# Performance work log

Measured on AMD Instinct MI355X. Metric: run time of the kernel, lower is better.

Reference implementation:

```python
import jax, jax.numpy as jnp
import numpy as np

B, N, D, R = 4, 2048, 1024, 64
LN_EPS = 1e-5


def setup_inputs() -> dict:
    key = jax.random.key(0)
    k_x, k_m, k_u, k_v = jax.random.split(key, 4)
    x = jax.random.normal(k_x, (B, N, D), dtype=jnp.float32)
    mask = jax.random.uniform(k_m, (B, N, R), dtype=jnp.float32)
    # xavier-style init for low-rank bases U_max, V_max: (d_model, R_max)
    scale = jnp.sqrt(2.0 / (D + R)).astype(jnp.float32)
    U = jax.random.normal(k_u, (D, R), dtype=jnp.float32) * scale
    V = jax.random.normal(k_v, (D, R), dtype=jnp.float32) * scale
    gamma = jnp.ones((D,), dtype=jnp.float32)
    beta = jnp.zeros((D,), dtype=jnp.float32)
    return {"x": x, "mask": mask, "U": U, "V": V, "gamma": gamma, "beta": beta}


def _layernorm(y, gamma, beta):
    mu = jnp.mean(y, axis=-1, keepdims=True)
    var = jnp.mean(jnp.square(y - mu), axis=-1, keepdims=True)
    return (y - mu) * jax.lax.rsqrt(var + LN_EPS) * gamma + beta


def reference(x, mask, U, V, gamma, beta):
    # Q/K: low-rank projections gated by per-token continuous mask
    Q = jnp.einsum('bnd,dr->bnr', x, U) * mask            # (B, N, R)
    K = jnp.einsum('bnd,dr->bnr', x, V) * mask            # (B, N, R)
    # effective rank per query token, clamped at 1
    r_eff = jnp.maximum(jnp.sum(mask, axis=-1, keepdims=True), 1.0)  # (B, N, 1)
    scores = jnp.einsum('bqr,bkr->bqk', Q, K) / jnp.sqrt(r_eff)      # (B, N, N)
    A = jax.nn.softmax(scores, axis=-1)
    delta = jnp.einsum('bqk,bkd->bqd', A, x)              # (B, N, D)
    # backbone is identity: out = LN(x + delta)
    return _layernorm(x + delta, gamma, beta)
```

## Files before the change

kernel.cpp:

```cpp
#include <hip/hip_runtime.h>

#define Bb 4
#define Nn 2048
#define Dd 1024
#define Rr 64
#define LN_EPS 1e-5f

typedef unsigned short u16;
typedef short bf16x8 __attribute__((ext_vector_type(8)));
typedef float f32x4 __attribute__((ext_vector_type(4)));

__device__ __forceinline__ u16 f2bf(float f) {
  unsigned u = __float_as_uint(f);
  u += 0x7FFFu + ((u >> 16) & 1u);
  return (u16)(u >> 16);
}

__device__ __forceinline__ void g2l16(u16* l, const u16* g) {
  __builtin_amdgcn_global_load_lds(
      (const __attribute__((address_space(1))) unsigned int*)g,
      (__attribute__((address_space(3))) unsigned int*)l, 16, 0, 0);
}

__global__ __launch_bounds__(256) void prep_x(const float* __restrict__ x,
                                              u16* __restrict__ xt) {
  __shared__ float tile[64][65];
  const int b = blockIdx.z;
  const int n0 = blockIdx.x * 64;
  const int d0 = blockIdx.y * 64;
  const int t = threadIdx.x;
  const int c = t & 63, r4 = t >> 6;
#pragma unroll
  for (int rr = 0; rr < 16; rr++) {
    int row = rr * 4 + r4;
    tile[row][c] = x[(size_t)(b * Nn + n0 + row) * Dd + d0 + c];
  }
  __syncthreads();
#pragma unroll
  for (int rr = 0; rr < 16; rr++) {
    int dd = rr * 4 + r4;
    xt[(size_t)(b * Dd + d0 + dd) * Nn + n0 + c] = f2bf(tile[c][dd]);
  }
}

__global__ __launch_bounds__(256) void prep_small(const float* __restrict__ U,
    const float* __restrict__ V, const float* __restrict__ mask,
    u16* __restrict__ uvt, float* __restrict__ qs) {
  if (blockIdx.x < 32) {
    __shared__ float tile[64][65];
    const int which = blockIdx.x >> 4;
    const int d0 = (blockIdx.x & 15) * 64;
    const float* src = which ? V : U;
    const int t = threadIdx.x, c = t & 63, r4 = t >> 6;
#pragma unroll
    for (int rr = 0; rr < 16; rr++) {
      int row = rr * 4 + r4;
      tile[row][c] = src[(size_t)(d0 + row) * Rr + c];
    }
    __syncthreads();
#pragma unroll
    for (int rr = 0; rr < 16; rr++) {
      int r = rr * 4 + r4;
      uvt[(size_t)(which * 64 + r) * Dd + d0 + c] = f2bf(tile[c][r]);
    }
  } else {
    const int row = (blockIdx.x - 32) * 4 + (threadIdx.x >> 6);
    const int lane = threadIdx.x & 63;
    float v = mask[(size_t)row * Rr + lane];
#pragma unroll
    for (int off = 32; off; off >>= 1) v += __shfl_xor(v, off);
    if (lane == 0) qs[row] = rsqrtf(fmaxf(v, 1.0f));
  }
}

__global__ __launch_bounds__(256) void proj_qk(const float* __restrict__ x,
    const float* __restrict__ mask, const u16* __restrict__ uvt,
    const float* __restrict__ qs,
    u16* __restrict__ Qo, u16* __restrict__ Ko) {
  const int t = threadIdx.x;
  const int w = t >> 6, l = t & 63, quad = l >> 4, l16 = l & 15;
  const int g0 = blockIdx.x * 32;
  f32x4 acc[2][2];
#pragma unroll
  for (int i = 0; i < 2; i++)
#pragma unroll
    for (int j = 0; j < 2; j++) acc[i][j] = (f32x4){0.f, 0.f, 0.f, 0.f};
  for (int k0 = 0; k0 < Dd; k0 += 32) {
    bf16x8 a[2];
#pragma unroll
    for (int mt = 0; mt < 2; mt++) {
      const float4* px = (const float4*)&x[(size_t)(g0 + mt * 16 + l16) * Dd + k0 + quad * 8];
      float4 x0 = px[0], x1 = px[1];
      bf16x8 av;
      av[0] = (short)f2bf(x0.x); av[1] = (short)f2bf(x0.y);
      av[2] = (short)f2bf(x0.z); av[3] = (short)f2bf(x0.w);
      av[4] = (short)f2bf(x1.x); av[5] = (short)f2bf(x1.y);
      av[6] = (short)f2bf(x1.z); av[7] = (short)f2bf(x1.w);
      a[mt] = av;
    }
    bf16x8 bfr[2];
#pragma unroll
    for (int i = 0; i < 2; i++) {
      int col = (w * 2 + i) * 16 + l16;
      bfr[i] = *(const bf16x8*)&uvt[(size_t)col * Dd + k0 + quad * 8];
    }
#pragma unroll
    for (int mt = 0; mt < 2; mt++)
#pragma unroll
      for (int i = 0; i < 2; i++)
        acc[mt][i] = __builtin_amdgcn_mfma_f32_16x16x32_bf16(a[mt], bfr[i], acc[mt][i], 0, 0, 0);
  }
#pragma unroll
  for (int mt = 0; mt < 2; mt++)
#pragma unroll
    for (int i = 0; i < 2; i++) {
      int col = (w * 2 + i) * 16 + l16;
      int r_ = col & 63;
#pragma unroll
      for (int r = 0; r < 4; r++) {
        int row = g0 + mt * 16 + quad * 4 + r;
        float v = acc[mt][i][r] * mask[(size_t)row * Rr + r_];
        if (col < 64) Qo[(size_t)row * Rr + r_] = f2bf(v * qs[row]);
        else          Ko[(size_t)row * Rr + r_] = f2bf(v);
      }
    }
}

__global__ __launch_bounds__(512, 2) void score_softmax(
    const u16* __restrict__ Qm, const u16* __restrict__ Km,
    u16* __restrict__ Pw, float* __restrict__ linv_g) {
  __shared__ float red[32][8];
  __shared__ float mfin[32];
  __shared__ u16 tsl[8][32][80];
  const int t = threadIdx.x;
  const int w = t >> 6, l = t & 63, quad = l >> 4, l16 = l & 15;
  const int id = blockIdx.x;
  const int xcd = id & 7;
  const int b = xcd >> 1;
  const int q0 = (((id >> 3) << 1) | (xcd & 1)) * 32;
  bf16x8 qf[2][2];
#pragma unroll
  for (int mt = 0; mt < 2; mt++)
#pragma unroll
    for (int ks = 0; ks < 2; ks++)
      qf[mt][ks] = *(const bf16x8*)&Qm[(size_t)(b * Nn + q0 + mt * 16 + l16) * Rr + ks * 32 + quad * 8];
  f32x4 acc[2][16];
#pragma unroll
  for (int mt = 0; mt < 2; mt++)
#pragma unroll
    for (int nt = 0; nt < 16; nt++) acc[mt][nt] = (f32x4){0.f, 0.f, 0.f, 0.f};
#pragma unroll
  for (int nt = 0; nt < 16; nt++) {
#pragma unroll
    for (int ks = 0; ks < 2; ks++) {
      bf16x8 kf = *(const bf16x8*)&Km[(size_t)(b * Nn + w * 256 + nt * 16 + l16) * Rr + ks * 32 + quad * 8];
#pragma unroll
      for (int mt = 0; mt < 2; mt++)
        acc[mt][nt] = __builtin_amdgcn_mfma_f32_16x16x32_bf16(qf[mt][ks], kf, acc[mt][nt], 0, 0, 0);
    }
  }
  float vmax[2][4];
#pragma unroll
  for (int mt = 0; mt < 2; mt++)
#pragma unroll
    for (int r = 0; r < 4; r++) {
      float m = -1e30f;
#pragma unroll
      for (int nt = 0; nt < 16; nt++) m = fmaxf(m, acc[mt][nt][r]);
#pragma unroll
      for (int off = 1; off < 16; off <<= 1) m = fmaxf(m, __shfl_xor(m, off));
      vmax[mt][r] = m;
    }
  if (l16 == 0) {
#pragma unroll
    for (int mt = 0; mt < 2; mt++)
#pragma unroll
      for (int r = 0; r < 4; r++) red[mt * 16 + quad * 4 + r][w] = vmax[mt][r];
  }
  __syncthreads();
  if (t < 32) {
    float m = -1e30f;
#pragma unroll
    for (int i = 0; i < 8; i++) m = fmaxf(m, red[t][i]);
    mfin[t] = m;
  }
  __syncthreads();
  float rowm[2][4], vsum[2][4];
#pragma unroll
  for (int mt = 0; mt < 2; mt++)
#pragma unroll
    for (int r = 0; r < 4; r++) {
      rowm[mt][r] = mfin[mt * 16 + quad * 4 + r];
      vsum[mt][r] = 0.f;
    }
#pragma unroll
  for (int mt = 0; mt < 2; mt++)
#pragma unroll
    for (int nt = 0; nt < 16; nt++)
#pragma unroll
      for (int r = 0; r < 4; r++) {
        float p = __expf(acc[mt][nt][r] - rowm[mt][r]);
        acc[mt][nt][r] = p;
        vsum[mt][r] += p;
      }
#pragma unroll
  for (int mt = 0; mt < 2; mt++)
#pragma unroll
    for (int r = 0; r < 4; r++) {
#pragma unroll
      for (int off = 1; off < 16; off <<= 1) vsum[mt][r] += __shfl_xor(vsum[mt][r], off);
    }
  __syncthreads();
  if (l16 == 0) {
#pragma unroll
    for (int mt = 0; mt < 2; mt++)
#pragma unroll
      for (int r = 0; r < 4; r++) red[mt * 16 + quad * 4 + r][w] = vsum[mt][r];
  }
  __syncthreads();
  if (t < 32) {
    float s = 0.f;
#pragma unroll
    for (int i = 0; i < 8; i++) s += red[t][i];
    linv_g[(size_t)b * Nn + q0 + t] = 1.f / s;
  }
#pragma unroll
  for (int c = 0; c < 4; c++) {
#pragma unroll
    for (int mt = 0; mt < 2; mt++)
#pragma unroll
      for (int i = 0; i < 4; i++) {
        const int nt = c * 4 + i;
#pragma unroll
        for (int r = 0; r < 4; r++)
          tsl[w][mt * 16 + quad * 4 + r][i * 16 + l16] = f2bf(acc[mt][nt][r]);
      }
#pragma unroll
    for (int it = 0; it < 4; it++) {
      const int u = it * 64 + l;
      const int row = u >> 3, cg = u & 7;
      bf16x8 vv = *(const bf16x8*)&tsl[w][row][cg * 8];
      *(bf16x8*)&Pw[((size_t)(b * Nn + q0 + row)) * Nn + w * 256 + c * 64 + cg * 8] = vv;
    }
  }
}

__global__ __launch_bounds__(256, 2) void pv_gemm(
    const u16* __restrict__ Pw, const u16* __restrict__ xt,
    const float* __restrict__ x, const float* __restrict__ linv_g,
    float* __restrict__ y) {
  __shared__ u16 As[128 * 64];
  __shared__ u16 Bs[128 * 64];
  const int t = threadIdx.x;
  const int w = t >> 6, l = t & 63, quad = l >> 4, l16 = l & 15;
  const int id = blockIdx.x;
  const int xcd = id & 7;
  const int b = xcd >> 1;
  const int nh = xcd & 1;
  const int rest = id >> 3;
  const int m0 = (rest & 15) * 128;
  const int n0 = (nh * 4 + (rest >> 4)) * 128;
  const int srow = w * 32 + (l >> 3);
  const int skoff = (((l & 7) ^ ((l >> 3) & 7)) * 8);
  f32x4 acc[4][4];
#pragma unroll
  for (int i = 0; i < 4; i++)
#pragma unroll
    for (int j = 0; j < 4; j++) acc[i][j] = (f32x4){0.f, 0.f, 0.f, 0.f};
  const int wm = w & 1, wn = w >> 1;
  const int sw = (l16 & 7);
  for (int k0 = 0; k0 < Nn; k0 += 64) {
    __syncthreads();
#pragma unroll
    for (int c = 0; c < 4; c++) {
      int row = srow + c * 8;
      g2l16(&As[(w * 32 + c * 8) * 64],
            &Pw[((size_t)(b * Nn + m0 + row)) * Nn + k0 + skoff]);
      g2l16(&Bs[(w * 32 + c * 8) * 64],
            &xt[((size_t)(b * Dd + n0 + row)) * Nn + k0 + skoff]);
    }
    __syncthreads();
#pragma unroll
    for (int ks = 0; ks < 2; ks++) {
      const int slot = ((ks * 4 + quad) ^ sw) * 8;
      bf16x8 af[4], bf_[4];
#pragma unroll
      for (int mt = 0; mt < 4; mt++)
        af[mt] = *(const bf16x8*)&As[(wm * 64 + mt * 16 + l16) * 64 + slot];
#pragma unroll
      for (int nt = 0; nt < 4; nt++)
        bf_[nt] = *(const bf16x8*)&Bs[(wn * 64 + nt * 16 + l16) * 64 + slot];
#pragma unroll
      for (int mt = 0; mt < 4; mt++)
#pragma unroll
        for (int nt = 0; nt < 4; nt++)
          acc[mt][nt] = __builtin_amdgcn_mfma_f32_16x16x32_bf16(af[mt], bf_[nt], acc[mt][nt], 0, 0, 0);
    }
  }
  float li[4][4];
#pragma unroll
  for (int mt = 0; mt < 4; mt++)
#pragma unroll
    for (int r = 0; r < 4; r++)
      li[mt][r] = linv_g[(size_t)b * Nn + m0 + wm * 64 + mt * 16 + quad * 4 + r];
#pragma unroll
  for (int mt = 0; mt < 4; mt++)
#pragma unroll
    for (int nt = 0; nt < 4; nt++) {
      const int nn = n0 + wn * 64 + nt * 16 + l16;
#pragma unroll
      for (int r = 0; r < 4; r++) {
        const int m = m0 + wm * 64 + mt * 16 + quad * 4 + r;
        const size_t off = ((size_t)(b * Nn + m)) * Dd + nn;
        y[off] = x[off] + li[mt][r] * acc[mt][nt][r];
      }
    }
}

__global__ __launch_bounds__(256) void ln_k(float* __restrict__ y,
    const float* __restrict__ gamma, const float* __restrict__ beta) {
  __shared__ float rs[4], rq[4];
  const int row = blockIdx.x;
  const int t = threadIdx.x;
  float* p = y + (size_t)row * Dd;
  float4 v = ((const float4*)p)[t];
  float s = v.x + v.y + v.z + v.w;
  float q = v.x * v.x + v.y * v.y + v.z * v.z + v.w * v.w;
#pragma unroll
  for (int off = 32; off; off >>= 1) {
    s += __shfl_xor(s, off);
    q += __shfl_xor(q, off);
  }
  if ((t & 63) == 0) { rs[t >> 6] = s; rq[t >> 6] = q; }
  __syncthreads();
  float S = rs[0] + rs[1] + rs[2] + rs[3];
  float Q2 = rq[0] + rq[1] + rq[2] + rq[3];
  float mu = S * (1.f / Dd);
  float var = Q2 * (1.f / Dd) - mu * mu;
  float rstd = rsqrtf(var + LN_EPS);
  float4 g = ((const float4*)gamma)[t];
  float4 be = ((const float4*)beta)[t];
  v.x = (v.x - mu) * rstd * g.x + be.x;
  v.y = (v.y - mu) * rstd * g.y + be.y;
  v.z = (v.z - mu) * rstd * g.z + be.z;
  v.w = (v.w - mu) * rstd * g.w + be.w;
  ((float4*)p)[t] = v;
}

extern "C" void kernel_launch(void* const* d_in, const int* in_sizes, int n_in,
                              void* d_out, int out_size, void* d_ws, size_t ws_size,
                              hipStream_t stream) {
  const float* x     = (const float*)d_in[0];
  const float* mask  = (const float*)d_in[1];
  const float* U     = (const float*)d_in[2];
  const float* V     = (const float*)d_in[3];
  const float* gamma = (const float*)d_in[4];
  const float* beta  = (const float*)d_in[5];
  float* out = (float*)d_out;
  char* ws = (char*)d_ws;
  u16*   xt   = (u16*)ws;
  u16*   Qw   = (u16*)(ws + (size_t)(16 << 20));
  u16*   Kw   = (u16*)(ws + (size_t)(17 << 20));
  u16*   uvt  = (u16*)(ws + (size_t)(18 << 20));
  float* qsb  = (float*)(ws + (size_t)(18 << 20) + (256 << 10));
  float* linv = (float*)(ws + (size_t)(18 << 20) + (288 << 10));
  u16*   Pw   = (u16*)(ws + (size_t)(19 << 20));

  prep_x       <<<dim3(Nn / 64, Dd / 64, Bb), 256, 0, stream>>>(x, xt);
  prep_small   <<<32 + (Bb * Nn) / 4, 256, 0, stream>>>(U, V, mask, uvt, qsb);
  proj_qk      <<<(Bb * Nn) / 32, 256, 0, stream>>>(x, mask, uvt, qsb, Qw, Kw);
  score_softmax<<<Bb * (Nn / 32), 512, 0, stream>>>(Qw, Kw, Pw, linv);
  pv_gemm      <<<Bb * (Nn / 128) * (Dd / 128), 256, 0, stream>>>(Pw, xt, x, linv, out);
  ln_k         <<<Bb * Nn, 256, 0, stream>>>(out, gamma, beta);
}
```

Measured before the change: 191.8 us.

## Shrink row tiles in projection and softmax, fuse qs into proj, one-wave LayerNorm rows

The mask row-sum and rsqrt scale move from a separate prep kernel into proj_qk, which now handles 16 rows per block and double-buffers its x and U/V register loads. score_softmax drops to 16 query rows per block with launch bounds raised to 4 blocks per CU, which lowers register pressure and doubles the block count. LayerNorm now assigns one wave per row and four rows per block, so the shared-memory reduction and block barrier are gone. The goal is more parallelism and occupancy in the small kernels and one fewer pass. The cost is that K fragments are reloaded from memory twice as often and grids get larger.

```diff
diff --git a/kernel.cpp b/kernel.cpp
--- a/kernel.cpp
+++ b/kernel.cpp
@@ -43,182 +43,166 @@
   }
 }
 
-__global__ __launch_bounds__(256) void prep_small(const float* __restrict__ U,
-    const float* __restrict__ V, const float* __restrict__ mask,
-    u16* __restrict__ uvt, float* __restrict__ qs) {
-  if (blockIdx.x < 32) {
-    __shared__ float tile[64][65];
-    const int which = blockIdx.x >> 4;
-    const int d0 = (blockIdx.x & 15) * 64;
-    const float* src = which ? V : U;
-    const int t = threadIdx.x, c = t & 63, r4 = t >> 6;
-#pragma unroll
-    for (int rr = 0; rr < 16; rr++) {
-      int row = rr * 4 + r4;
-      tile[row][c] = src[(size_t)(d0 + row) * Rr + c];
-    }
-    __syncthreads();
-#pragma unroll
-    for (int rr = 0; rr < 16; rr++) {
-      int r = rr * 4 + r4;
-      uvt[(size_t)(which * 64 + r) * Dd + d0 + c] = f2bf(tile[c][r]);
-    }
-  } else {
-    const int row = (blockIdx.x - 32) * 4 + (threadIdx.x >> 6);
-    const int lane = threadIdx.x & 63;
-    float v = mask[(size_t)row * Rr + lane];
-#pragma unroll
-    for (int off = 32; off; off >>= 1) v += __shfl_xor(v, off);
-    if (lane == 0) qs[row] = rsqrtf(fmaxf(v, 1.0f));
+__global__ __launch_bounds__(256) void prep_uv(const float* __restrict__ U,
+    const float* __restrict__ V, u16* __restrict__ uvt) {
+  __shared__ float tile[64][65];
+  const int which = blockIdx.x >> 4;
+  const int d0 = (blockIdx.x & 15) * 64;
+  const float* src = which ? V : U;
+  const int t = threadIdx.x, c = t & 63, r4 = t >> 6;
+#pragma unroll
+  for (int rr = 0; rr < 16; rr++) {
+    int row = rr * 4 + r4;
+    tile[row][c] = src[(size_t)(d0 + row) * Rr + c];
+  }
+  __syncthreads();
+#pragma unroll
+  for (int rr = 0; rr < 16; rr++) {
+    int r = rr * 4 + r4;
+    uvt[(size_t)(which * 64 + r) * Dd + d0 + c] = f2bf(tile[c][r]);
   }
 }
 
 __global__ __launch_bounds__(256) void proj_qk(const float* __restrict__ x,
     const float* __restrict__ mask, const u16* __restrict__ uvt,
-    const float* __restrict__ qs,
     u16* __restrict__ Qo, u16* __restrict__ Ko) {
+  __shared__ float qsl[16];
   const int t = threadIdx.x;
   const int w = t >> 6, l = t & 63, quad = l >> 4, l16 = l & 15;
-  const int g0 = blockIdx.x * 32;
-  f32x4 acc[2][2];
-#pragma unroll
-  for (int i = 0; i < 2; i++)
-#pragma unroll
-    for (int j = 0; j < 2; j++) acc[i][j] = (f32x4){0.f, 0.f, 0.f, 0.f};
+  const int g0 = blockIdx.x * 16;
+#pragma unroll
+  for (int it = 0; it < 4; it++) {
+    const int row = it * 4 + w;
+    float v = mask[(size_t)(g0 + row) * Rr + l];
+#pragma unroll
+    for (int off = 32; off; off >>= 1) v += __shfl_xor(v, off);
+    if (l == 0) qsl[row] = rsqrtf(fmaxf(v, 1.0f));
+  }
+  f32x4 acc[2];
+  acc[0] = (f32x4){0.f, 0.f, 0.f, 0.f};
+  acc[1] = (f32x4){0.f, 0.f, 0.f, 0.f};
+  bf16x8 a_cur, b_cur[2];
+  {
+    const float4* px = (const float4*)&x[(size_t)(g0 + l16) * Dd + quad * 8];
+    float4 x0 = px[0], x1 = px[1];
+    a_cur[0] = (short)f2bf(x0.x); a_cur[1] = (short)f2bf(x0.y);
+    a_cur[2] = (short)f2bf(x0.z); a_cur[3] = (short)f2bf(x0.w);
+    a_cur[4] = (short)f2bf(x1.x); a_cur[5] = (short)f2bf(x1.y);
+    a_cur[6] = (short)f2bf(x1.z); a_cur[7] = (short)f2bf(x1.w);
+#pragma unroll
+    for (int i = 0; i < 2; i++) {
+      int col = w * 32 + i * 16 + l16;
+      b_cur[i] = *(const bf16x8*)&uvt[(size_t)col * Dd + quad * 8];
+    }
+  }
   for (int k0 = 0; k0 < Dd; k0 += 32) {
-    bf16x8 a[2];
-#pragma unroll
-    for (int mt = 0; mt < 2; mt++) {
-      const float4* px = (const float4*)&x[(size_t)(g0 + mt * 16 + l16) * Dd + k0 + quad * 8];
+    const int k1 = (k0 + 32 < Dd) ? k0 + 32 : 0;
+    bf16x8 a_nxt, b_nxt[2];
+    {
+      const float4* px = (const float4*)&x[(size_t)(g0 + l16) * Dd + k1 + quad * 8];
       float4 x0 = px[0], x1 = px[1];
-      bf16x8 av;
-      av[0] = (short)f2bf(x0.x); av[1] = (short)f2bf(x0.y);
-      av[2] = (short)f2bf(x0.z); av[3] = (short)f2bf(x0.w);
-      av[4] = (short)f2bf(x1.x); av[5] = (short)f2bf(x1.y);
-      av[6] = (short)f2bf(x1.z); av[7] = (short)f2bf(x1.w);
-      a[mt] = av;
-    }
-    bf16x8 bfr[2];
-#pragma unroll
-    for (int i = 0; i < 2; i++) {
-      int col = (w * 2 + i) * 16 + l16;
-      bfr[i] = *(const bf16x8*)&uvt[(size_t)col * Dd + k0 + quad * 8];
-    }
-#pragma unroll
-    for (int mt = 0; mt < 2; mt++)
-#pragma unroll
-      for (int i = 0; i < 2; i++)
-        acc[mt][i] = __builtin_amdgcn_mfma_f32_16x16x32_bf16(a[mt], bfr[i], acc[mt][i], 0, 0, 0);
-  }
-#pragma unroll
-  for (int mt = 0; mt < 2; mt++)
-#pragma unroll
-    for (int i = 0; i < 2; i++) {
-      int col = (w * 2 + i) * 16 + l16;
-      int r_ = col & 63;
-#pragma unroll
-      for (int r = 0; r < 4; r++) {
-        int row = g0 + mt * 16 + quad * 4 + r;
-        float v = acc[mt][i][r] * mask[(size_t)row * Rr + r_];
-        if (col < 64) Qo[(size_t)row * Rr + r_] = f2bf(v * qs[row]);
-        else          Ko[(size_t)row * Rr + r_] = f2bf(v);
+      a_nxt[0] = (short)f2bf(x0.x); a_nxt[1] = (short)f2bf(x0.y);
+      a_nxt[2] = (short)f2bf(x0.z); a_nxt[3] = (short)f2bf(x0.w);
+      a_nxt[4] = (short)f2bf(x1.x); a_nxt[5] = (short)f2bf(x1.y);
+      a_nxt[6] = (short)f2bf(x1.z); a_nxt[7] = (short)f2bf(x1.w);
+#pragma unroll
+      for (int i = 0; i < 2; i++) {
+        int col = w * 32 + i * 16 + l16;
+        b_nxt[i] = *(const bf16x8*)&uvt[(size_t)col * Dd + k1 + quad * 8];
       }
     }
-}
-
-__global__ __launch_bounds__(512, 2) void score_softmax(
+#pragma unroll
+    for (int i = 0; i < 2; i++)
+      acc[i] = __builtin_amdgcn_mfma_f32_16x16x32_bf16(a_cur, b_cur[i], acc[i], 0, 0, 0);
+    a_cur = a_nxt; b_cur[0] = b_nxt[0]; b_cur[1] = b_nxt[1];
+  }
+  __syncthreads();
+#pragma unroll
+  for (int i = 0; i < 2; i++) {
+    const int col = w * 32 + i * 16 + l16;
+    const int r_ = col & 63;
+#pragma unroll
+    for (int r = 0; r < 4; r++) {
+      const int rl = quad * 4 + r;
+      const int row = g0 + rl;
+      float v = acc[i][r] * mask[(size_t)row * Rr + r_];
+      if (col < 64) Qo[(size_t)row * Rr + r_] = f2bf(v * qsl[rl]);
+      else          Ko[(size_t)row * Rr + r_] = f2bf(v);
+    }
+  }
+}
+
+__global__ __launch_bounds__(512, 4) void score_softmax(
     const u16* __restrict__ Qm, const u16* __restrict__ Km,
     u16* __restrict__ Pw, float* __restrict__ linv_g) {
-  __shared__ float red[32][8];
-  __shared__ float mfin[32];
-  __shared__ u16 tsl[8][32][80];
+  __shared__ float red[16][8];
+  __shared__ float mfin[16];
+  __shared__ u16 tsl[8][16][72];
   const int t = threadIdx.x;
   const int w = t >> 6, l = t & 63, quad = l >> 4, l16 = l & 15;
   const int id = blockIdx.x;
   const int xcd = id & 7;
   const int b = xcd >> 1;
-  const int q0 = (((id >> 3) << 1) | (xcd & 1)) * 32;
-  bf16x8 qf[2][2];
-#pragma unroll
-  for (int mt = 0; mt < 2; mt++)
-#pragma unroll
-    for (int ks = 0; ks < 2; ks++)
-      qf[mt][ks] = *(const bf16x8*)&Qm[(size_t)(b * Nn + q0 + mt * 16 + l16) * Rr + ks * 32 + quad * 8];
-  f32x4 acc[2][16];
-#pragma unroll
-  for (int mt = 0; mt < 2; mt++)
-#pragma unroll
-    for (int nt = 0; nt < 16; nt++) acc[mt][nt] = (f32x4){0.f, 0.f, 0.f, 0.f};
+  const int q0 = (((id >> 3) << 1) | (xcd & 1)) * 16;
+  bf16x8 qf[2];
+#pragma unroll
+  for (int ks = 0; ks < 2; ks++)
+    qf[ks] = *(const bf16x8*)&Qm[(size_t)(b * Nn + q0 + l16) * Rr + ks * 32 + quad * 8];
+  f32x4 acc[16];
+#pragma unroll
+  for (int nt = 0; nt < 16; nt++) acc[nt] = (f32x4){0.f, 0.f, 0.f, 0.f};
 #pragma unroll
   for (int nt = 0; nt < 16; nt++) {
 #pragma unroll
     for (int ks = 0; ks < 2; ks++) {
       bf16x8 kf = *(const bf16x8*)&Km[(size_t)(b * Nn + w * 256 + nt * 16 + l16) * Rr + ks * 32 + quad * 8];
-#pragma unroll
-      for (int mt = 0; mt < 2; mt++)
-        acc[mt][nt] = __builtin_amdgcn_mfma_f32_16x16x32_bf16(qf[mt][ks], kf, acc[mt][nt], 0, 0, 0);
-    }
-  }
-  float vmax[2][4];
-#pragma unroll
-  for (int mt = 0; mt < 2; mt++)
-#pragma unroll
-    for (int r = 0; r < 4; r++) {
-      float m = -1e30f;
-#pragma unroll
-      for (int nt = 0; nt < 16; nt++) m = fmaxf(m, acc[mt][nt][r]);
-#pragma unroll
-      for (int off = 1; off < 16; off <<= 1) m = fmaxf(m, __shfl_xor(m, off));
-      vmax[mt][r] = m;
-    }
+      acc[nt] = __builtin_amdgcn_mfma_f32_16x16x32_bf16(qf[ks], kf, acc[nt], 0, 0, 0);
+    }
+  }
+  float vmax[4];
+#pragma unroll
+  for (int r = 0; r < 4; r++) {
+    float m = -1e30f;
+#pragma unroll
+    for (int nt = 0; nt < 16; nt++) m = fmaxf(m, acc[nt][r]);
+#pragma unroll
+    for (int off = 1; off < 16; off <<= 1) m = fmaxf(m, __shfl_xor(m, off));
+    vmax[r] = m;
+  }
   if (l16 == 0) {
 #pragma unroll
-    for (int mt = 0; mt < 2; mt++)
-#pragma unroll
-      for (int r = 0; r < 4; r++) red[mt * 16 + quad * 4 + r][w] = vmax[mt][r];
-  }
-  __syncthreads();
-  if (t < 32) {
+    for (int r = 0; r < 4; r++) red[quad * 4 + r][w] = vmax[r];
+  }
+  __syncthreads();
+  if (t < 16) {
     float m = -1e30f;
 #pragma unroll
     for (int i = 0; i < 8; i++) m = fmaxf(m, red[t][i]);
     mfin[t] = m;
   }
   __syncthreads();
-  float rowm[2][4], vsum[2][4];
-#pragma unroll
-  for (int mt = 0; mt < 2; mt++)
+  float rowm[4], vsum[4];
+#pragma unroll
+  for (int r = 0; r < 4; r++) { rowm[r] = mfin[quad * 4 + r]; vsum[r] = 0.f; }
+#pragma unroll
+  for (int nt = 0; nt < 16; nt++)
 #pragma unroll
     for (int r = 0; r < 4; r++) {
-      rowm[mt][r] = mfin[mt * 16 + quad * 4 + r];
-      vsum[mt][r] = 0.f;
-    }
-#pragma unroll
-  for (int mt = 0; mt < 2; mt++)
-#pragma unroll
-    for (int nt = 0; nt < 16; nt++)
-#pragma unroll
-      for (int r = 0; r < 4; r++) {
-        float p = __expf(acc[mt][nt][r] - rowm[mt][r]);
-        acc[mt][nt][r] = p;
-        vsum[mt][r] += p;
-      }
-#pragma unroll
-  for (int mt = 0; mt < 2; mt++)
-#pragma unroll
-    for (int r = 0; r < 4; r++) {
-#pragma unroll
-      for (int off = 1; off < 16; off <<= 1) vsum[mt][r] += __shfl_xor(vsum[mt][r], off);
-    }
-  __syncthreads();
+      float p = __expf(acc[nt][r] - rowm[r]);
+      acc[nt][r] = p;
+      vsum[r] += p;
+    }
+#pragma unroll
+  for (int r = 0; r < 4; r++) {
+#pragma unroll
+    for (int off = 1; off < 16; off <<= 1) vsum[r] += __shfl_xor(vsum[r], off);
+  }
   if (l16 == 0) {
 #pragma unroll
-    for (int mt = 0; mt < 2; mt++)
-#pragma unroll
-      for (int r = 0; r < 4; r++) red[mt * 16 + quad * 4 + r][w] = vsum[mt][r];
-  }
-  __syncthreads();
-  if (t < 32) {
+    for (int r = 0; r < 4; r++) red[quad * 4 + r][w] = vsum[r];
+  }
+  __syncthreads();
+  if (t < 16) {
     float s = 0.f;
 #pragma unroll
     for (int i = 0; i < 8; i++) s += red[t][i];
@@ -227,16 +211,14 @@
 #pragma unroll
   for (int c = 0; c < 4; c++) {
 #pragma unroll
-    for (int mt = 0; mt < 2; mt++)
-#pragma unroll
-      for (int i = 0; i < 4; i++) {
-        const int nt = c * 4 + i;
-#pragma unroll
-        for (int r = 0; r < 4; r++)
-          tsl[w][mt * 16 + quad * 4 + r][i * 16 + l16] = f2bf(acc[mt][nt][r]);
-      }
-#pragma unroll
-    for (int it = 0; it < 4; it++) {
+    for (int i = 0; i < 4; i++) {
+      const int nt = c * 4 + i;
+#pragma unroll
+      for (int r = 0; r < 4; r++)
+        tsl[w][quad * 4 + r][i * 16 + l16] = f2bf(acc[nt][r]);
+    }
+#pragma unroll
+    for (int it = 0; it < 2; it++) {
       const int u = it * 64 + l;
       const int row = u >> 3, cg = u & 7;
       bf16x8 vv = *(const bf16x8*)&tsl[w][row][cg * 8];
@@ -319,32 +301,36 @@
 
 __global__ __launch_bounds__(256) void ln_k(float* __restrict__ y,
     const float* __restrict__ gamma, const float* __restrict__ beta) {
-  __shared__ float rs[4], rq[4];
-  const int row = blockIdx.x;
-  const int t = threadIdx.x;
+  const int t = threadIdx.x, w = t >> 6, lane = t & 63;
+  const int row = blockIdx.x * 4 + w;
   float* p = y + (size_t)row * Dd;
-  float4 v = ((const float4*)p)[t];
-  float s = v.x + v.y + v.z + v.w;
-  float q = v.x * v.x + v.y * v.y + v.z * v.z + v.w * v.w;
+  float4 v[4];
+  float s = 0.f, q = 0.f;
+#pragma unroll
+  for (int i = 0; i < 4; i++) {
+    v[i] = ((const float4*)p)[i * 64 + lane];
+    s += v[i].x + v[i].y + v[i].z + v[i].w;
+    q += v[i].x * v[i].x + v[i].y * v[i].y + v[i].z * v[i].z + v[i].w * v[i].w;
+  }
 #pragma unroll
   for (int off = 32; off; off >>= 1) {
     s += __shfl_xor(s, off);
     q += __shfl_xor(q, off);
   }
-  if ((t & 63) == 0) { rs[t >> 6] = s; rq[t >> 6] = q; }
-  __syncthreads();
-  float S = rs[0] + rs[1] + rs[2] + rs[3];
-  float Q2 = rq[0] + rq[1] + rq[2] + rq[3];
-  float mu = S * (1.f / Dd);
-  float var = Q2 * (1.f / Dd) - mu * mu;
-  float rstd = rsqrtf(var + LN_EPS);
-  float4 g = ((const float4*)gamma)[t];
-  float4 be = ((const float4*)beta)[t];
-  v.x = (v.x - mu) * rstd * g.x + be.x;
-  v.y = (v.y - mu) * rstd * g.y + be.y;
-  v.z = (v.z - mu) * rstd * g.z + be.z;
-  v.w = (v.w - mu) * rstd * g.w + be.w;
-  ((float4*)p)[t] = v;
+  const float mu = s * (1.f / Dd);
+  const float var = q * (1.f / Dd) - mu * mu;
+  const float rstd = rsqrtf(var + LN_EPS);
+#pragma unroll
+  for (int i = 0; i < 4; i++) {
+    float4 g = ((const float4*)gamma)[i * 64 + lane];
+    float4 be = ((const float4*)beta)[i * 64 + lane];
+    float4 o;
+    o.x = (v[i].x - mu) * rstd * g.x + be.x;
+    o.y = (v[i].y - mu) * rstd * g.y + be.y;
+    o.z = (v[i].z - mu) * rstd * g.z + be.z;
+    o.w = (v[i].w - mu) * rstd * g.w + be.w;
+    ((float4*)p)[i * 64 + lane] = o;
+  }
 }
 
 extern "C" void kernel_launch(void* const* d_in, const int* in_sizes, int n_in,
@@ -362,14 +348,13 @@
   u16*   Qw   = (u16*)(ws + (size_t)(16 << 20));
   u16*   Kw   = (u16*)(ws + (size_t)(17 << 20));
   u16*   uvt  = (u16*)(ws + (size_t)(18 << 20));
-  float* qsb  = (float*)(ws + (size_t)(18 << 20) + (256 << 10));
   float* linv = (float*)(ws + (size_t)(18 << 20) + (288 << 10));
   u16*   Pw   = (u16*)(ws + (size_t)(19 << 20));
 
+  prep_uv      <<<32, 256, 0, stream>>>(U, V, uvt);
   prep_x       <<<dim3(Nn / 64, Dd / 64, Bb), 256, 0, stream>>>(x, xt);
-  prep_small   <<<32 + (Bb * Nn) / 4, 256, 0, stream>>>(U, V, mask, uvt, qsb);
-  proj_qk      <<<(Bb * Nn) / 32, 256, 0, stream>>>(x, mask, uvt, qsb, Qw, Kw);
-  score_softmax<<<Bb * (Nn / 32), 512, 0, stream>>>(Qw, Kw, Pw, linv);
+  proj_qk      <<<(Bb * Nn) / 16, 256, 0, stream>>>(x, mask, uvt, Qw, Kw);
+  score_softmax<<<Bb * (Nn / 16), 512, 0, stream>>>(Qw, Kw, Pw, linv);
   pv_gemm      <<<Bb * (Nn / 128) * (Dd / 128), 256, 0, stream>>>(Pw, xt, x, linv, out);
-  ln_k         <<<Bb * Nn, 256, 0, stream>>>(out, gamma, beta);
-}
+  ln_k         <<<(Bb * Nn) / 4, 256, 0, stream>>>(out, gamma, beta);
+}
```

Result: slower. 202.6 us (+5.6%).
